# Performance work log

Hardware: AMD Instinct MI355X
Metric: run time of the kernel (lower is better)

The kernel has to match this reference:

```python
import jax, jax.numpy as jnp
import numpy as np

MAX_BITS = 256.0  # 2**8


def _quantize_kernel(kern):
    # ConfigurableDense.quantize(): symmetric 8-bit fake-quantization of the kernel.
    # qmin starts at 1e10, qmax at -1e10, so first call uses min/max of kernel.
    qmin = jnp.minimum(jnp.float32(1e10), jnp.min(kern))
    qmax = jnp.maximum(jnp.float32(-1e10), jnp.max(kern))
    s = 2.0 * jnp.maximum(jnp.abs(qmin), jnp.abs(qmax)) / MAX_BITS
    return jnp.round(kern / s) * s


def setup_inputs() -> dict:
    key = jax.random.key(0)
    ks = jax.random.split(key, 9)
    B, S, D_IN, D_MODEL = 4, 2048, 1024, 1024
    sc = 0.02
    return {
        "q": jax.random.normal(ks[0], (B, S, D_IN), jnp.float32),
        "k": jax.random.normal(ks[1], (B, S, D_IN), jnp.float32),
        "v": jax.random.normal(ks[2], (B, S, D_IN), jnp.float32),
        "Wq": jax.random.normal(ks[3], (D_IN, D_MODEL), jnp.float32) * sc,
        "bq": jax.random.normal(ks[4], (D_MODEL,), jnp.float32) * sc,
        "Wk": jax.random.normal(ks[5], (D_IN, D_MODEL), jnp.float32) * sc,
        "bk": jax.random.normal(ks[6], (D_MODEL,), jnp.float32) * sc,
        "Wv": jax.random.normal(ks[7], (D_IN, D_MODEL), jnp.float32) * sc,
        "bv": jax.random.normal(ks[8], (D_MODEL,), jnp.float32) * sc,
    }


def reference(q, k, v, Wq, bq, Wk, bk, Wv, bv):
    # Projections with fake-quantized kernels (ConfigurableDense, activation=None).
    qp = jnp.einsum('bsi,id->bsd', q, _quantize_kernel(Wq)) + bq
    kp = jnp.einsum('bsi,id->bsd', k, _quantize_kernel(Wk)) + bk
    vp = jnp.einsum('bsi,id->bsd', v, _quantize_kernel(Wv)) + bv
    # MovingAverageQuantizers are identity on the first call (steps=0 < warmup).
    dk = jnp.float32(kp.shape[-1])
    logits = jnp.einsum('bqd,bkd->bqk', qp, kp) / jnp.sqrt(dk)  # [B, S, S]
    attn = jax.nn.softmax(logits, axis=-1)
    return jnp.einsum('bqk,bkd->bqd', attn, vp)
```

## Files before the change

### kernel.cpp

```cpp
#include <hip/hip_runtime.h>
#include <stdint.h>


typedef unsigned short ushort_t;
typedef __attribute__((ext_vector_type(8))) short short8;
typedef __bf16 bf16x8 __attribute__((ext_vector_type(8)));
typedef __attribute__((ext_vector_type(4))) float floatx4;

__device__ __forceinline__ ushort_t f2bf(float x) {
  unsigned u = __float_as_uint(x);
  unsigned r = (u + 0x7fffu + ((u >> 16) & 1u)) >> 16;
  return (ushort_t)r;
}
__device__ __forceinline__ float bf2f(ushort_t u) {
  return __uint_as_float(((unsigned)u) << 16);
}

__device__ __forceinline__ void gl_lds16(const ushort_t* g, ushort_t* l) {
  __builtin_amdgcn_global_load_lds(
      (const __attribute__((address_space(1))) unsigned int*)g,
      (__attribute__((address_space(3))) unsigned int*)l, 16, 0, 0);
}

#define BM 128
#define BN 128
#define BK 64

template <int CMODE>
__global__ __launch_bounds__(256, 2) void gemm_bt(
    const ushort_t* __restrict__ A, const ushort_t* __restrict__ Bt,
    void* __restrict__ Cv, const float* __restrict__ bias0,
    const float* __restrict__ bias1, const float* __restrict__ bias2, int K,
    int ldc, float alpha, long strideA, long strideB, long strideC) {
  __shared__ __attribute__((aligned(16))) ushort_t sA[BM * BK];
  __shared__ __attribute__((aligned(16))) ushort_t sB[BN * BK];

  const int t = threadIdx.x;
  const int lane = t & 63;
  const int wave = t >> 6;
  const int bn = blockIdx.x, bm = blockIdx.y, bz = blockIdx.z;

  const ushort_t* Ab = A + (long)bz * strideA;
  const ushort_t* Bb = Bt + (long)bz * strideB;

  const long a_row0 = (long)bm * BM;
  const long b_row0 = (long)bn * BN;

  const int crow = t >> 3;
  const int schunk = (t & 7) ^ (crow & 7);

  const ushort_t* gA = Ab + (a_row0 + crow) * (long)K + schunk * 8;
  const ushort_t* gB = Bb + (b_row0 + crow) * (long)K + schunk * 8;

  ushort_t* lA = sA + wave * 512;
  ushort_t* lB = sB + wave * 512;

  floatx4 acc[4][4];
#pragma unroll
  for (int i = 0; i < 4; ++i)
#pragma unroll
    for (int j = 0; j < 4; ++j) acc[i][j] = {0.f, 0.f, 0.f, 0.f};

  const int wm = (wave & 1) * 64;
  const int wn = (wave >> 1) * 64;
  const int fr = lane & 15;
  const int fg = lane >> 4;

  int offA[2][4], offB[2][4];
#pragma unroll
  for (int s = 0; s < 2; ++s)
#pragma unroll
    for (int i = 0; i < 4; ++i) {
      int rowA = wm + i * 16 + fr;
      int rowB = wn + i * 16 + fr;
      int cg = s * 4 + fg;
      offA[s][i] = rowA * BK + ((cg ^ (rowA & 7)) * 8);
      offB[s][i] = rowB * BK + ((cg ^ (rowB & 7)) * 8);
    }

  for (int k0 = 0; k0 < K; k0 += BK) {
#pragma unroll
    for (int i = 0; i < 4; ++i) {
      gl_lds16(gA + (long)i * 32 * K, lA + i * 2048);
      gl_lds16(gB + (long)i * 32 * K, lB + i * 2048);
    }
    gA += BK;
    gB += BK;
    __syncthreads();

#pragma unroll
    for (int s = 0; s < 2; ++s) {
      bf16x8 af[4], bfr[4];
#pragma unroll
      for (int i = 0; i < 4; ++i) {
        af[i] = *(const bf16x8*)&sA[offA[s][i]];
        bfr[i] = *(const bf16x8*)&sB[offB[s][i]];
      }
#pragma unroll
      for (int mi = 0; mi < 4; ++mi)
#pragma unroll
        for (int ni = 0; ni < 4; ++ni)
          acc[mi][ni] = __builtin_amdgcn_mfma_f32_16x16x32_bf16(
              af[mi], bfr[ni], acc[mi][ni], 0, 0, 0);
    }
    __syncthreads();
  }

  const int r0 = fg * 4;
  const int cc = fr;
  const float* bias = (CMODE == 3) ? (bz == 0 ? bias0 : (bz == 1 ? bias1 : bias2))
                                   : bias0;
  const bool tstore = (CMODE == 1) || (CMODE == 3 && bz == 2);
  ushort_t* Cz16 = (ushort_t*)Cv + (long)bz * strideC;
  float* Cz32 = (float*)Cv + (long)bz * strideC;

#pragma unroll
  for (int mi = 0; mi < 4; ++mi) {
#pragma unroll
    for (int ni = 0; ni < 4; ++ni) {
      long gm0 = a_row0 + wm + mi * 16 + r0;
      long gn = b_row0 + wn + ni * 16 + cc;
      float vv[4];
#pragma unroll
      for (int r = 0; r < 4; ++r) {
        vv[r] = acc[mi][ni][r] * alpha;
        if (bias) vv[r] += bias[gn];
      }
      if (CMODE == 2) {
#pragma unroll
        for (int r = 0; r < 4; ++r) Cz32[(gm0 + r) * ldc + gn] = vv[r];
      } else if (tstore) {
        long b = gm0 >> 11, s = gm0 & 2047;
        ushort4 u4;
        u4.x = f2bf(vv[0]); u4.y = f2bf(vv[1]);
        u4.z = f2bf(vv[2]); u4.w = f2bf(vv[3]);
        *(ushort4*)&Cz16[b * (2048L * 1024L) + gn * 2048L + s] = u4;
      } else {
#pragma unroll
        for (int r = 0; r < 4; ++r) Cz16[(gm0 + r) * ldc + gn] = f2bf(vv[r]);
      }
    }
  }
}

__global__ __launch_bounds__(256) void absmax_k(
    const float* __restrict__ W0, const float* __restrict__ W1,
    const float* __restrict__ W2, unsigned* __restrict__ outv) {
  const float* W = blockIdx.z == 0 ? W0 : (blockIdx.z == 1 ? W1 : W2);
  float m = 0.f;
  const long n = 1024L * 1024L;
  for (long i = (long)blockIdx.x * blockDim.x + threadIdx.x; i < n;
       i += (long)gridDim.x * blockDim.x)
    m = fmaxf(m, fabsf(W[i]));
  for (int off = 32; off; off >>= 1) m = fmaxf(m, __shfl_xor(m, off));
  __shared__ float red[4];
  int lane = threadIdx.x & 63, wave = threadIdx.x >> 6;
  if (lane == 0) red[wave] = m;
  __syncthreads();
  if (threadIdx.x == 0) {
    m = fmaxf(fmaxf(red[0], red[1]), fmaxf(red[2], red[3]));
    atomicMax(&outv[blockIdx.z], __float_as_uint(m));
  }
}

__global__ __launch_bounds__(256) void quant_w_k(
    const float* __restrict__ W0, const float* __restrict__ W1,
    const float* __restrict__ W2, const unsigned* __restrict__ scales,
    ushort_t* __restrict__ Wt) {
  const int z = blockIdx.z;
  const float* W = z == 0 ? W0 : (z == 1 ? W1 : W2);
  const float s = __uint_as_float(scales[z]) * (1.0f / 128.0f);
  __shared__ float tile[32][33];
  const int tx = threadIdx.x & 31, ty = threadIdx.x >> 5;
  const int k0 = blockIdx.y * 32, n0 = blockIdx.x * 32;
#pragma unroll
  for (int i = 0; i < 4; ++i)
    tile[ty + i * 8][tx] = W[(long)(k0 + ty + i * 8) * 1024 + n0 + tx];
  __syncthreads();
  ushort_t* wt = Wt + (long)z * 1024 * 1024;
#pragma unroll
  for (int i = 0; i < 4; ++i) {
    float w = tile[tx][ty + i * 8];
    float qv = rintf(w / s) * s;
    wt[(long)(n0 + ty + i * 8) * 1024 + k0 + tx] = f2bf(qv);
  }
}

__global__ __launch_bounds__(256) void cast3_k(
    const float* __restrict__ q, const float* __restrict__ k,
    const float* __restrict__ v, ushort_t* __restrict__ qb,
    ushort_t* __restrict__ kb, ushort_t* __restrict__ vb) {
  const int z = blockIdx.z;
  const float4* src = (const float4*)(z == 0 ? q : (z == 1 ? k : v));
  ushort_t* dst = z == 0 ? qb : (z == 1 ? kb : vb);
  const long nv = (4L * 2048 * 1024) / 4;
  for (long i = (long)blockIdx.x * blockDim.x + threadIdx.x; i < nv;
       i += (long)gridDim.x * blockDim.x) {
    float4 f = src[i];
    ushort4 u4;
    u4.x = f2bf(f.x); u4.y = f2bf(f.y); u4.z = f2bf(f.z); u4.w = f2bf(f.w);
    *(ushort4*)(dst + i * 4) = u4;
  }
}

__global__ __launch_bounds__(256) void softmax_k(ushort_t* __restrict__ P) {
  const long row = blockIdx.x;
  ushort_t* p = P + row * 2048;
  const int t = threadIdx.x;
  const int lane = t & 63, wave = t >> 6;
  short8 v8 = *(const short8*)&p[t * 8];
  float x[8];
#pragma unroll
  for (int j = 0; j < 8; ++j) x[j] = bf2f((ushort_t)v8[j]);
  float m = x[0];
#pragma unroll
  for (int j = 1; j < 8; ++j) m = fmaxf(m, x[j]);
  for (int off = 32; off; off >>= 1) m = fmaxf(m, __shfl_xor(m, off));
  __shared__ float rmax[4], rsum[4];
  if (lane == 0) rmax[wave] = m;
  __syncthreads();
  m = fmaxf(fmaxf(rmax[0], rmax[1]), fmaxf(rmax[2], rmax[3]));
  float s = 0.f;
#pragma unroll
  for (int j = 0; j < 8; ++j) {
    x[j] = __expf(x[j] - m);
    s += x[j];
  }
  for (int off = 32; off; off >>= 1) s += __shfl_xor(s, off);
  if (lane == 0) rsum[wave] = s;
  __syncthreads();
  s = rsum[0] + rsum[1] + rsum[2] + rsum[3];
  float inv = 1.0f / s;
  short8 o8;
#pragma unroll
  for (int j = 0; j < 8; ++j) o8[j] = (short)f2bf(x[j] * inv);
  *(short8*)&p[t * 8] = o8;
}

extern "C" void kernel_launch(void* const* d_in, const int* in_sizes, int n_in,
                              void* d_out, int out_size, void* d_ws,
                              size_t ws_size, hipStream_t stream) {
  const float* q = (const float*)d_in[0];
  const float* k = (const float*)d_in[1];
  const float* v = (const float*)d_in[2];
  const float* Wq = (const float*)d_in[3];
  const float* bq = (const float*)d_in[4];
  const float* Wk = (const float*)d_in[5];
  const float* bk = (const float*)d_in[6];
  const float* Wv = (const float*)d_in[7];
  const float* bv = (const float*)d_in[8];
  float* out = (float*)d_out;
  char* ws = (char*)d_ws;

  unsigned* scales = (unsigned*)ws;
  ushort_t* Wt = (ushort_t*)(ws + 256);
  ushort_t* qb = (ushort_t*)(ws + 6291712);
  ushort_t* kb = qb + 8388608;
  ushort_t* vb = kb + 8388608;
  ushort_t* qp = vb + 8388608;
  ushort_t* kp = qp + 8388608;
  ushort_t* vpT = kp + 8388608;
  ushort_t* P = qb;

  hipMemsetAsync(scales, 0, 64, stream);
  absmax_k<<<dim3(64, 1, 3), 256, 0, stream>>>(Wq, Wk, Wv, scales);
  quant_w_k<<<dim3(32, 32, 3), 256, 0, stream>>>(Wq, Wk, Wv, scales, Wt);
  cast3_k<<<dim3(512, 1, 3), 256, 0, stream>>>(q, k, v, qb, kb, vb);

  gemm_bt<3><<<dim3(8, 64, 3), 256, 0, stream>>>(
      qb, Wt, qp, bq, bk, bv, 1024, 1024, 1.0f, 8388608L, 1048576L, 8388608L);

  gemm_bt<0><<<dim3(16, 16, 4), 256, 0, stream>>>(
      qp, kp, P, nullptr, nullptr, nullptr, 1024, 2048, 0.03125f, 2097152L,
      2097152L, 4194304L);

  softmax_k<<<8192, 256, 0, stream>>>(P);

  gemm_bt<2><<<dim3(8, 16, 4), 256, 0, stream>>>(
      P, vpT, out, nullptr, nullptr, nullptr, 2048, 1024, 1.0f, 4194304L,
      2097152L, 2097152L);
}
```

Baseline: 353.9 us.

## Compute QK^T logits in FP8 with scaled MFMA and swap grid mapping

The projection GEMM now writes Q and K projections as FP8 (e4m3) bytes instead of bf16. A new qk_fp8 kernel computes the logits with the 16x16x128 f8f6f4 scaled MFMA at unit scale, which halves operand bytes and doubles math throughput per instruction. The grid for the projection and PV GEMMs is also swapped so that blockIdx.x indexes M tiles, changing the tile launch order for L2 reuse. FP8 logits lose precision and may push error past tolerance.

```diff
diff --git a/kernel.cpp b/kernel.cpp
--- a/kernel.cpp
+++ b/kernel.cpp
@@ -6,6 +6,7 @@
 typedef __attribute__((ext_vector_type(8))) short short8;
 typedef __bf16 bf16x8 __attribute__((ext_vector_type(8)));
 typedef __attribute__((ext_vector_type(4))) float floatx4;
+typedef __attribute__((ext_vector_type(8))) int int8v;
 
 __device__ __forceinline__ ushort_t f2bf(float x) {
   unsigned u = __float_as_uint(x);
@@ -15,8 +16,11 @@
 __device__ __forceinline__ float bf2f(ushort_t u) {
   return __uint_as_float(((unsigned)u) << 16);
 }
-
-__device__ __forceinline__ void gl_lds16(const ushort_t* g, ushort_t* l) {
+__device__ __forceinline__ unsigned char f2fp8(float x) {
+  return (unsigned char)(__builtin_amdgcn_cvt_pk_fp8_f32(x, x, 0, false) & 0xff);
+}
+
+__device__ __forceinline__ void gl_lds16(const void* g, void* l) {
   __builtin_amdgcn_global_load_lds(
       (const __attribute__((address_space(1))) unsigned int*)g,
       (__attribute__((address_space(3))) unsigned int*)l, 16, 0, 0);
@@ -26,19 +30,22 @@
 #define BN 128
 #define BK 64
 
-template <int CMODE>
+template <int CMODE, int SWAP>
 __global__ __launch_bounds__(256, 2) void gemm_bt(
     const ushort_t* __restrict__ A, const ushort_t* __restrict__ Bt,
-    void* __restrict__ Cv, const float* __restrict__ bias0,
-    const float* __restrict__ bias1, const float* __restrict__ bias2, int K,
-    int ldc, float alpha, long strideA, long strideB, long strideC) {
+    void* __restrict__ Cv, void* __restrict__ Cv8,
+    const float* __restrict__ bias0, const float* __restrict__ bias1,
+    const float* __restrict__ bias2, int K, int ldc, float alpha, long strideA,
+    long strideB, long strideC) {
   __shared__ __attribute__((aligned(16))) ushort_t sA[BM * BK];
   __shared__ __attribute__((aligned(16))) ushort_t sB[BN * BK];
 
   const int t = threadIdx.x;
   const int lane = t & 63;
   const int wave = t >> 6;
-  const int bn = blockIdx.x, bm = blockIdx.y, bz = blockIdx.z;
+  const int bm = SWAP ? blockIdx.x : blockIdx.y;
+  const int bn = SWAP ? blockIdx.y : blockIdx.x;
+  const int bz = blockIdx.z;
 
   const ushort_t* Ab = A + (long)bz * strideA;
   const ushort_t* Bb = Bt + (long)bz * strideB;
@@ -108,11 +115,11 @@
 
   const int r0 = fg * 4;
   const int cc = fr;
-  const float* bias = (CMODE == 3) ? (bz == 0 ? bias0 : (bz == 1 ? bias1 : bias2))
-                                   : bias0;
-  const bool tstore = (CMODE == 1) || (CMODE == 3 && bz == 2);
-  ushort_t* Cz16 = (ushort_t*)Cv + (long)bz * strideC;
+  const float* bias =
+      (CMODE == 3) ? (bz == 0 ? bias0 : (bz == 1 ? bias1 : bias2)) : bias0;
   float* Cz32 = (float*)Cv + (long)bz * strideC;
+  unsigned char* C8 = (unsigned char*)Cv8 + (long)bz * 8388608L;
+  ushort_t* CvpT = (ushort_t*)Cv;
 
 #pragma unroll
   for (int mi = 0; mi < 4; ++mi) {
@@ -129,18 +136,105 @@
       if (CMODE == 2) {
 #pragma unroll
         for (int r = 0; r < 4; ++r) Cz32[(gm0 + r) * ldc + gn] = vv[r];
-      } else if (tstore) {
+      } else if (CMODE == 3 && bz == 2) {
         long b = gm0 >> 11, s = gm0 & 2047;
         ushort4 u4;
         u4.x = f2bf(vv[0]); u4.y = f2bf(vv[1]);
         u4.z = f2bf(vv[2]); u4.w = f2bf(vv[3]);
-        *(ushort4*)&Cz16[b * (2048L * 1024L) + gn * 2048L + s] = u4;
+        *(ushort4*)&CvpT[b * (2048L * 1024L) + gn * 2048L + s] = u4;
       } else {
 #pragma unroll
-        for (int r = 0; r < 4; ++r) Cz16[(gm0 + r) * ldc + gn] = f2bf(vv[r]);
+        for (int r = 0; r < 4; ++r) C8[(gm0 + r) * 1024 + gn] = f2fp8(vv[r]);
       }
     }
   }
+}
+
+__global__ __launch_bounds__(256, 2) void qk_fp8(
+    const unsigned char* __restrict__ Q8, const unsigned char* __restrict__ K8,
+    ushort_t* __restrict__ P) {
+  __shared__ __attribute__((aligned(16))) unsigned char sA[128 * 128];
+  __shared__ __attribute__((aligned(16))) unsigned char sB[128 * 128];
+  const int t = threadIdx.x;
+  const int lane = t & 63, wave = t >> 6;
+  const int bm = blockIdx.x, bn = blockIdx.y, bz = blockIdx.z;
+
+  const unsigned char* Ab = Q8 + (long)bz * 2097152L + (long)bm * 128 * 1024;
+  const unsigned char* Bb = K8 + (long)bz * 2097152L + (long)bn * 128 * 1024;
+
+  const int crow = t >> 3;
+  const int schunk = (t & 7) ^ (crow & 7);
+  const unsigned char* gA = Ab + crow * 1024 + schunk * 16;
+  const unsigned char* gB = Bb + crow * 1024 + schunk * 16;
+  unsigned char* lA = sA + wave * 1024;
+  unsigned char* lB = sB + wave * 1024;
+
+  floatx4 acc[4][4];
+#pragma unroll
+  for (int i = 0; i < 4; ++i)
+#pragma unroll
+    for (int j = 0; j < 4; ++j) acc[i][j] = {0.f, 0.f, 0.f, 0.f};
+
+  const int wm = (wave & 1) * 64;
+  const int wn = (wave >> 1) * 64;
+  const int fr = lane & 15;
+  const int fg = lane >> 4;
+
+  int offA[4][2], offB[4][2];
+#pragma unroll
+  for (int i = 0; i < 4; ++i) {
+    int rA = wm + i * 16 + fr;
+    int rB = wn + i * 16 + fr;
+    offA[i][0] = rA * 128 + (((2 * fg) ^ (rA & 7)) * 16);
+    offA[i][1] = rA * 128 + (((2 * fg + 1) ^ (rA & 7)) * 16);
+    offB[i][0] = rB * 128 + (((2 * fg) ^ (rB & 7)) * 16);
+    offB[i][1] = rB * 128 + (((2 * fg + 1) ^ (rB & 7)) * 16);
+  }
+
+  for (int k0 = 0; k0 < 1024; k0 += 128) {
+#pragma unroll
+    for (int i = 0; i < 4; ++i) {
+      gl_lds16(gA + (long)i * 32 * 1024, lA + i * 4096);
+      gl_lds16(gB + (long)i * 32 * 1024, lB + i * 4096);
+    }
+    gA += 128;
+    gB += 128;
+    __syncthreads();
+
+    int8v af[4], bfr[4];
+#pragma unroll
+    for (int i = 0; i < 4; ++i) {
+      int4 lo = *(const int4*)&sA[offA[i][0]];
+      int4 hi = *(const int4*)&sA[offA[i][1]];
+      af[i][0] = lo.x; af[i][1] = lo.y; af[i][2] = lo.z; af[i][3] = lo.w;
+      af[i][4] = hi.x; af[i][5] = hi.y; af[i][6] = hi.z; af[i][7] = hi.w;
+      int4 lo2 = *(const int4*)&sB[offB[i][0]];
+      int4 hi2 = *(const int4*)&sB[offB[i][1]];
+      bfr[i][0] = lo2.x; bfr[i][1] = lo2.y; bfr[i][2] = lo2.z; bfr[i][3] = lo2.w;
+      bfr[i][4] = hi2.x; bfr[i][5] = hi2.y; bfr[i][6] = hi2.z; bfr[i][7] = hi2.w;
+    }
+#pragma unroll
+    for (int mi = 0; mi < 4; ++mi)
+#pragma unroll
+      for (int ni = 0; ni < 4; ++ni)
+        acc[mi][ni] = __builtin_amdgcn_mfma_scale_f32_16x16x128_f8f6f4(
+            af[mi], bfr[ni], acc[mi][ni], 0, 0, 0, 127, 0, 127);
+    __syncthreads();
+  }
+
+  const int r0 = fg * 4;
+  const int cc = fr;
+#pragma unroll
+  for (int mi = 0; mi < 4; ++mi)
+#pragma unroll
+    for (int ni = 0; ni < 4; ++ni)
+#pragma unroll
+      for (int r = 0; r < 4; ++r) {
+        long gm = (long)bm * 128 + wm + mi * 16 + r0 + r;
+        long gn = (long)bn * 128 + wn + ni * 16 + cc;
+        P[(long)bz * 4194304L + gm * 2048 + gn] =
+            f2bf(acc[mi][ni][r] * 0.03125f);
+      }
 }
 
 __global__ __launch_bounds__(256) void absmax_k(
@@ -257,26 +351,24 @@
   ushort_t* qb = (ushort_t*)(ws + 6291712);
   ushort_t* kb = qb + 8388608;
   ushort_t* vb = kb + 8388608;
-  ushort_t* qp = vb + 8388608;
-  ushort_t* kp = qp + 8388608;
-  ushort_t* vpT = kp + 8388608;
   ushort_t* P = qb;
+  ushort_t* vpT = (ushort_t*)(ws + 73400576);
+  unsigned char* qp8 = (unsigned char*)(ws + 90177792);
+  unsigned char* kp8 = (unsigned char*)(ws + 98566400);
 
   hipMemsetAsync(scales, 0, 64, stream);
   absmax_k<<<dim3(64, 1, 3), 256, 0, stream>>>(Wq, Wk, Wv, scales);
   quant_w_k<<<dim3(32, 32, 3), 256, 0, stream>>>(Wq, Wk, Wv, scales, Wt);
   cast3_k<<<dim3(512, 1, 3), 256, 0, stream>>>(q, k, v, qb, kb, vb);
 
-  gemm_bt<3><<<dim3(8, 64, 3), 256, 0, stream>>>(
-      qb, Wt, qp, bq, bk, bv, 1024, 1024, 1.0f, 8388608L, 1048576L, 8388608L);
-
-  gemm_bt<0><<<dim3(16, 16, 4), 256, 0, stream>>>(
-      qp, kp, P, nullptr, nullptr, nullptr, 1024, 2048, 0.03125f, 2097152L,
-      2097152L, 4194304L);
+  gemm_bt<3, 1><<<dim3(64, 8, 3), 256, 0, stream>>>(
+      qb, Wt, vpT, qp8, bq, bk, bv, 1024, 1024, 1.0f, 8388608L, 1048576L, 0L);
+
+  qk_fp8<<<dim3(16, 16, 4), 256, 0, stream>>>(qp8, kp8, P);
 
   softmax_k<<<8192, 256, 0, stream>>>(P);
 
-  gemm_bt<2><<<dim3(8, 16, 4), 256, 0, stream>>>(
-      P, vpT, out, nullptr, nullptr, nullptr, 2048, 1024, 1.0f, 4194304L,
-      2097152L, 2097152L);
-}
+  gemm_bt<2, 1><<<dim3(16, 8, 4), 256, 0, stream>>>(
+      P, vpT, out, nullptr, nullptr, nullptr, nullptr, 2048, 1024, 1.0f,
+      4194304L, 2097152L, 2097152L);
+}
```

New measurement: 314.5 us. -11.1%, faster.
